# Performance work log

Measured on AMD Instinct MI355X. Metric: run time of the kernel, lower is better.

## Reference

```python
import jax, jax.numpy as jnp
import numpy as np

# FlowNetC correlation hyperparameters (match init_kwargs)
PAD = 20          # pad_size
KSIZE = 1         # kernel_size (1x1 patches -> plain per-pixel dot over channels)
MAXD = 20         # max_displacement
STRIDE1 = 1       # output grid stride
STRIDE2 = 2       # displacement stride


def setup_inputs() -> dict:
    key = jax.random.key(0)
    k1, k2 = jax.random.split(key)
    B, C, H, W = 16, 256, 48, 64
    return {
        "input1": jax.random.normal(k1, (B, C, H, W), dtype=jnp.float32),
        "input2": jax.random.normal(k2, (B, C, H, W), dtype=jnp.float32),
    }


def _correlation(in1, in2):
    B, C, H, W = in1.shape
    # pad input2 spatially; max_displacement == pad_size so every shifted
    # window of size (H, W) stays in-bounds of the padded map.
    pad2 = jnp.pad(in2, ((0, 0), (0, 0), (PAD, PAD), (PAD, PAD)))
    disps = np.arange(-MAXD, MAXD + 1, STRIDE2)  # 21 offsets per axis
    offsets = jnp.asarray(
        [(PAD + dy, PAD + dx) for dy in disps for dx in disps], dtype=jnp.int32
    )  # [D=441, 2]

    in1s = in1[:, :, ::STRIDE1, ::STRIDE1]  # output-grid view of input1

    def one_displacement(off):
        # shifted (H, W) window of padded input2 at displacement (dy, dx)
        sl = jax.lax.dynamic_slice(pad2, (0, 0, off[0], off[1]), (B, C, H, W))
        sl = sl[:, :, ::STRIDE1, ::STRIDE1]
        # per-pixel dot product over channels
        return jnp.einsum('bchw,bchw->bhw', in1s, sl)

    # lax.map keeps memory low: one [B,C,H,W] slice live at a time
    out = jax.lax.map(one_displacement, offsets)  # [D, B, Ho, Wo]
    sumelems = KSIZE * KSIZE * C  # CUDA kernel normalizes by patch elem count
    return jnp.transpose(out, (1, 0, 2, 3)) / sumelems  # [B, D, Ho, Wo]


def reference(input1, input2):
    return _correlation(input1, input2)
```

## Files before the change

kernel.cpp:

```cpp
#include <hip/hip_runtime.h>
#include <stdint.h>

#define NB 16
#define NC 256
#define NH 48
#define NW 64
#define ND 21
#define HW (NH * NW)
#define ROW_ELEMS (NW * NC)
#define SOUT_LD (NW + 1)
#define SOUT_SZ (ND * SOUT_LD)
#define NXCD 8
#define NWG (NB * NH)

typedef __bf16 bf16x8 __attribute__((ext_vector_type(8)));
typedef float f32x4 __attribute__((ext_vector_type(4)));

__device__ __forceinline__ int xcd_wg(int orig) {
    return (orig & (NXCD - 1)) * (NWG / NXCD) + (orig >> 3);
}

__device__ __forceinline__ int sw_addr(int x, int chunk) {
    int cs = (chunk & ~7) | ((chunk ^ x) & 7);
    return x * 256 + (cs << 3);
}
__device__ __forceinline__ int posx(int x) { return ((x & 1) << 5) | (x >> 1); }

__device__ __forceinline__ bf16x8 load_pack8(const float* __restrict__ p, int cbase) {
    bf16x8 v;
#pragma unroll
    for (int j = 0; j < 8; ++j)
        v[j] = (__bf16)p[(size_t)(cbase + j) * HW];
    return v;
}

__global__ void __launch_bounds__(256, 4)
convert_in2(const float* __restrict__ in2, unsigned short* __restrict__ ws) {
    __shared__ unsigned short s[ROW_ELEMS];
    const int tid = threadIdx.x;
    const int wg = xcd_wg(blockIdx.x);
    const int b = wg / NH, y = wg % NH;
    const int x = tid & 63, g0 = tid >> 6;
    const int px = posx(x);
    const float* p = in2 + ((size_t)b * NC * NH + y) * NW + x;
#pragma unroll
    for (int i = 0; i < 8; ++i) {
        const int chunk = g0 * 8 + i;
        bf16x8 v = load_pack8(p, chunk * 8);
        *(bf16x8*)&s[sw_addr(px, chunk)] = v;
    }
    __syncthreads();
    unsigned short* wr = ws + ((size_t)b * NH + y) * ROW_ELEMS;
#pragma unroll
    for (int i = 0; i < 8; ++i) {
        const int e = (i * 256 + tid) * 8;
        *(bf16x8*)(wr + e) = *(const bf16x8*)(s + e);
    }
}

__global__ void __launch_bounds__(256, 3)
corr_main(const float* __restrict__ in1, const unsigned short* __restrict__ ws,
          float* __restrict__ out) {
    __shared__ unsigned short s1[ROW_ELEMS];
    __shared__ float sout[2 * SOUT_SZ];
    const int tid  = threadIdx.x;
    const int wg   = xcd_wg(blockIdx.x);
    const int b    = wg / NH, y = wg % NH;
    const int lane = tid & 63, wave = tid >> 6;
    const int m_lo = lane & 15, quad = lane >> 4;
    const int par  = wave & 1, nt = wave >> 1;

    {
        const int x = tid & 63, g0 = tid >> 6;
        const int px = posx(x);
        const float* p = in1 + ((size_t)b * NC * NH + y) * NW + x;
#pragma unroll
        for (int i = 0; i < 8; ++i) {
            const int chunk = g0 * 8 + i;
            bf16x8 v = load_pack8(p, chunk * 8);
            *(bf16x8*)&s1[sw_addr(px, chunk)] = v;
        }
    }
    for (int i = tid; i < 2 * SOUT_SZ; i += 256) sout[i] = 0.0f;

    const int d0 = (y >= 20) ? 0 : (21 - y) >> 1;
    const int d1 = min(20, (67 - y) >> 1);
    const unsigned short* wsb = ws + (size_t)b * NH * ROW_ELEMS;
    const int bpos = par * 32 + 16 * nt + m_lo;

    auto load_b = [&](bf16x8 (&bf)[8], int dyi) {
        const unsigned short* row = wsb + (size_t)(y - 20 + 2 * dyi) * ROW_ELEMS;
#pragma unroll
        for (int kb = 0; kb < 8; ++kb)
            bf[kb] = *(const bf16x8*)&row[sw_addr(bpos, 4 * kb + quad)];
    };

    bf16x8 bfA[8], bfB[8];
    load_b(bfA, d0);
    __syncthreads();

    bf16x8 afrag[2][8];
#pragma unroll
    for (int mm = 0; mm < 2; ++mm) {
        const int pos = par * 32 + 16 * mm + m_lo;
#pragma unroll
        for (int kb = 0; kb < 8; ++kb)
            afrag[mm][kb] = *(const bf16x8*)&s1[sw_addr(pos, 4 * kb + quad)];
    }

    float* outbase = out + (((size_t)b * (ND * ND)) * NH + (size_t)y) * NW;
    for (int dyi = 0; dyi < ND; ++dyi) {
        if (dyi >= d0 && dyi <= d1) continue;
        float* ob = outbase + (size_t)dyi * ND * HW;
        for (int i = tid; i < ND * NW; i += 256)
            __builtin_nontemporal_store(0.0f, &ob[(size_t)(i >> 6) * HW + (i & 63)]);
    }

    const float scale = 1.0f / 256.0f;
    const int xq  = 4 * quad;
    const int xph = 16 * nt + m_lo;

    auto step = [&](bf16x8 (&bc)[8], bf16x8 (&bn)[8], int dyi, int cb) {
        if (dyi < d1) load_b(bn, dyi + 1);

        f32x4 acc0 = {0.f, 0.f, 0.f, 0.f}, acc1 = {0.f, 0.f, 0.f, 0.f};
#pragma unroll
        for (int kb = 0; kb < 8; ++kb) {
            acc0 = __builtin_amdgcn_mfma_f32_16x16x32_bf16(afrag[0][kb], bc[kb], acc0, 0, 0, 0);
            acc1 = __builtin_amdgcn_mfma_f32_16x16x32_bf16(afrag[1][kb], bc[kb], acc1, 0, 0, 0);
        }

        float* sb = sout + cb * SOUT_SZ;
#pragma unroll
        for (int r = 0; r < 4; ++r) {
            {
                const int xh = xq + r;
                const int dxi = xph - xh + 10;
                if ((unsigned)dxi <= 20u) sb[dxi * SOUT_LD + 2 * xh + par] = acc0[r];
            }
            {
                const int xh = 16 + xq + r;
                const int dxi = xph - xh + 10;
                if ((unsigned)dxi <= 20u) sb[dxi * SOUT_LD + 2 * xh + par] = acc1[r];
            }
        }
        if (dyi > d0) {
            float* sp = sout + (cb ^ 1) * SOUT_SZ;
            float* ob = outbase + (size_t)(dyi - 1) * ND * HW;
            for (int i = tid; i < ND * NW; i += 256) {
                const int pl = i >> 6, x = i & 63;
                float v = sp[pl * SOUT_LD + x];
                __builtin_nontemporal_store(v * scale, &ob[(size_t)pl * HW + x]);
                sp[pl * SOUT_LD + x] = 0.0f;
            }
        }
        __asm__ __volatile__("s_waitcnt lgkmcnt(0)\n\ts_barrier" ::: "memory");
    };

    int dyi = d0, last;
    while (true) {
        step(bfA, bfB, dyi, 0);
        if (++dyi > d1) { last = 0; break; }
        step(bfB, bfA, dyi, 1);
        if (++dyi > d1) { last = 1; break; }
    }
    {
        float* sp = sout + last * SOUT_SZ;
        float* ob = outbase + (size_t)d1 * ND * HW;
        for (int i = tid; i < ND * NW; i += 256) {
            const int pl = i >> 6, x = i & 63;
            __builtin_nontemporal_store(sp[pl * SOUT_LD + x] * scale, &ob[(size_t)pl * HW + x]);
        }
    }
}

__global__ void __launch_bounds__(256, 2)
corr_fallback(const float* __restrict__ in1, const float* __restrict__ in2,
              float* __restrict__ out) {
    __shared__ unsigned short s1[ROW_ELEMS];
    __shared__ unsigned short s2[ROW_ELEMS];
    const int tid = threadIdx.x;
    const int b = blockIdx.x / NH, y = blockIdx.x % NH;
    const int lane = tid & 63, wave = tid >> 6;
    const int m_lo = lane & 15, quad = lane >> 4;
    const int asub = wave >> 1, bsub = wave & 1;
    {
        const int x = tid & 63, g0 = tid >> 6;
        const float* p = in1 + ((size_t)b * NC * NH + y) * NW + x;
        for (int i = 0; i < 8; ++i) {
            const int chunk = g0 * 8 + i;
            bf16x8 v = load_pack8(p, chunk * 8);
            *(bf16x8*)&s1[sw_addr(x, chunk)] = v;
        }
    }
    __syncthreads();
    bf16x8 afrag[2][8];
    for (int mm = 0; mm < 2; ++mm) {
        const int x = 32 * asub + 16 * mm + m_lo;
        for (int kb = 0; kb < 8; ++kb)
            afrag[mm][kb] = *(const bf16x8*)&s1[sw_addr(x, 4 * kb + quad)];
    }
    const float scale = 1.0f / 256.0f;
    for (int dyi = 0; dyi < ND; ++dyi) {
        const int ys = y + 2 * dyi - 20;
        float* ob = out + (((size_t)b * (ND * ND) + (size_t)dyi * ND) * NH + y) * NW;
        if ((unsigned)ys >= (unsigned)NH) {
            for (int i = tid; i < ND * NW; i += 256)
                ob[(size_t)(i >> 6) * HW + (i & 63)] = 0.0f;
            continue;
        }
        __syncthreads();
        {
            const int x = tid & 63, g0 = tid >> 6;
            const float* p = in2 + ((size_t)b * NC * NH + ys) * NW + x;
            for (int i = 0; i < 8; ++i) {
                const int chunk = g0 * 8 + i;
                bf16x8 v = load_pack8(p, chunk * 8);
                *(bf16x8*)&s2[sw_addr(x, chunk)] = v;
            }
        }
        __syncthreads();
        f32x4 acc[2][2];
        for (int mm = 0; mm < 2; ++mm)
            for (int nn = 0; nn < 2; ++nn) acc[mm][nn] = (f32x4){0.f, 0.f, 0.f, 0.f};
        for (int nn = 0; nn < 2; ++nn) {
            const int xpp = 32 * bsub + 16 * nn + m_lo;
            for (int kb = 0; kb < 8; ++kb) {
                bf16x8 bfrag = *(const bf16x8*)&s2[sw_addr(xpp, 4 * kb + quad)];
                acc[0][nn] = __builtin_amdgcn_mfma_f32_16x16x32_bf16(afrag[0][kb], bfrag, acc[0][nn], 0, 0, 0);
                acc[1][nn] = __builtin_amdgcn_mfma_f32_16x16x32_bf16(afrag[1][kb], bfrag, acc[1][nn], 0, 0, 0);
            }
        }
        for (int mm = 0; mm < 2; ++mm)
            for (int nn = 0; nn < 2; ++nn) {
                const int xb = 32 * asub + 16 * mm + 4 * quad;
                const int xpp = 32 * bsub + 16 * nn + m_lo;
                for (int r = 0; r < 4; ++r) {
                    const int x = xb + r, d = xpp - x;
                    if (d >= -20 && d <= 20 && !(d & 1))
                        ob[(size_t)((d + 20) >> 1) * HW + x] = acc[mm][nn][r] * scale;
                }
            }
        for (int i = tid; i < ND * 20; i += 256) {
            const int dxi = i / 20, j = i - dxi * 20;
            const int dx = 2 * dxi - 20, a = dx < 0 ? -dx : dx;
            if (j < a) {
                const int x = dx < 0 ? j : (NW - dx + j);
                ob[(size_t)dxi * HW + x] = 0.0f;
            }
        }
    }
}

extern "C" void kernel_launch(void* const* d_in, const int* in_sizes, int n_in,
                              void* d_out, int out_size, void* d_ws, size_t ws_size,
                              hipStream_t stream) {
    const float* in1 = (const float*)d_in[0];
    const float* in2 = (const float*)d_in[1];
    float* out = (float*)d_out;
    const size_t need = (size_t)NB * NH * ROW_ELEMS * sizeof(unsigned short);
    if (ws_size >= need) {
        convert_in2<<<dim3(NWG), dim3(256), 0, stream>>>(in2, (unsigned short*)d_ws);
        corr_main<<<dim3(NWG), dim3(256), 0, stream>>>(in1, (const unsigned short*)d_ws, out);
    } else {
        corr_fallback<<<dim3(NWG), dim3(256), 0, stream>>>(in1, in2, out);
    }
}
```

Before: 60.11 us.

## Store bf16 workspace in MFMA fragment order and overlap output drain with MFMAs

```diff
diff --git a/kernel.cpp b/kernel.cpp
--- a/kernel.cpp
+++ b/kernel.cpp
@@ -26,6 +26,10 @@
 }
 __device__ __forceinline__ int posx(int x) { return ((x & 1) << 5) | (x >> 1); }
 
+__device__ __forceinline__ int frag_off(int w, int kb, int l) {
+    return w * 4096 + kb * 512 + ((l ^ ((w & 3) << 1)) << 3);
+}
+
 __device__ __forceinline__ bf16x8 load_pack8(const float* __restrict__ p, int cbase) {
     bf16x8 v;
 #pragma unroll
@@ -41,13 +45,16 @@
     const int wg = xcd_wg(blockIdx.x);
     const int b = wg / NH, y = wg % NH;
     const int x = tid & 63, g0 = tid >> 6;
-    const int px = posx(x);
+    const int par = x & 1, m_lo = (x >> 1) & 15, nt = x >> 5;
+    const int w = (nt << 1) | par;
     const float* p = in2 + ((size_t)b * NC * NH + y) * NW + x;
 #pragma unroll
     for (int i = 0; i < 8; ++i) {
         const int chunk = g0 * 8 + i;
+        const int kb = chunk >> 2, quad = chunk & 3;
+        const int l = (quad << 4) | m_lo;
         bf16x8 v = load_pack8(p, chunk * 8);
-        *(bf16x8*)&s[sw_addr(px, chunk)] = v;
+        *(bf16x8*)&s[frag_off(w, kb, l)] = v;
     }
     __syncthreads();
     unsigned short* wr = ws + ((size_t)b * NH + y) * ROW_ELEMS;
@@ -86,13 +93,13 @@
     const int d0 = (y >= 20) ? 0 : (21 - y) >> 1;
     const int d1 = min(20, (67 - y) >> 1);
     const unsigned short* wsb = ws + (size_t)b * NH * ROW_ELEMS;
-    const int bpos = par * 32 + 16 * nt + m_lo;
+    const int slice_off = frag_off(wave, 0, lane);
 
     auto load_b = [&](bf16x8 (&bf)[8], int dyi) {
-        const unsigned short* row = wsb + (size_t)(y - 20 + 2 * dyi) * ROW_ELEMS;
+        const unsigned short* row = wsb + (size_t)(y - 20 + 2 * dyi) * ROW_ELEMS + slice_off;
 #pragma unroll
         for (int kb = 0; kb < 8; ++kb)
-            bf[kb] = *(const bf16x8*)&row[sw_addr(bpos, 4 * kb + quad)];
+            bf[kb] = *(const bf16x8*)&row[kb * 512];
     };
 
     bf16x8 bfA[8], bfB[8];
@@ -119,15 +126,39 @@
     const float scale = 1.0f / 256.0f;
     const int xq  = 4 * quad;
     const int xph = 16 * nt + m_lo;
+    const int dx0 = tid & 63;
+    const int dp0 = tid >> 6;
 
     auto step = [&](bf16x8 (&bc)[8], bf16x8 (&bn)[8], int dyi, int cb) {
         if (dyi < d1) load_b(bn, dyi + 1);
+
+        const bool have = dyi > d0;
+        float dv[6];
+        float* sp = sout + (cb ^ 1) * SOUT_SZ;
+        if (have) {
+#pragma unroll
+            for (int k = 0; k < 6; ++k) {
+                const int i = dx0 + (dp0 + 4 * k) * 64;
+                if (i < ND * NW) dv[k] = sp[(dp0 + 4 * k) * SOUT_LD + dx0];
+            }
+        }
 
         f32x4 acc0 = {0.f, 0.f, 0.f, 0.f}, acc1 = {0.f, 0.f, 0.f, 0.f};
 #pragma unroll
         for (int kb = 0; kb < 8; ++kb) {
             acc0 = __builtin_amdgcn_mfma_f32_16x16x32_bf16(afrag[0][kb], bc[kb], acc0, 0, 0, 0);
             acc1 = __builtin_amdgcn_mfma_f32_16x16x32_bf16(afrag[1][kb], bc[kb], acc1, 0, 0, 0);
+        }
+
+        if (have) {
+            float* ob = outbase + (size_t)(dyi - 1) * ND * HW;
+#pragma unroll
+            for (int k = 0; k < 6; ++k) {
+                const int i = dx0 + (dp0 + 4 * k) * 64;
+                if (i < ND * NW)
+                    __builtin_nontemporal_store(dv[k] * scale,
+                                                &ob[(size_t)(dp0 + 4 * k) * HW + dx0]);
+            }
         }
 
         float* sb = sout + cb * SOUT_SZ;
@@ -142,16 +173,6 @@
                 const int xh = 16 + xq + r;
                 const int dxi = xph - xh + 10;
                 if ((unsigned)dxi <= 20u) sb[dxi * SOUT_LD + 2 * xh + par] = acc1[r];
-            }
-        }
-        if (dyi > d0) {
-            float* sp = sout + (cb ^ 1) * SOUT_SZ;
-            float* ob = outbase + (size_t)(dyi - 1) * ND * HW;
-            for (int i = tid; i < ND * NW; i += 256) {
-                const int pl = i >> 6, x = i & 63;
-                float v = sp[pl * SOUT_LD + x];
-                __builtin_nontemporal_store(v * scale, &ob[(size_t)pl * HW + x]);
-                sp[pl * SOUT_LD + x] = 0.0f;
             }
         }
         __asm__ __volatile__("s_waitcnt lgkmcnt(0)\n\ts_barrier" ::: "memory");
```

After: 55.74 us. -7.3%, faster.
